# Kernel tuning notes

Hardware: AMD Instinct MI355X
Metric: run time of the kernel (lower is better)

## Reference

```python
import jax, jax.numpy as jnp
import numpy as np

N, C, E, H = 10000, 128, 640000, 8


def setup_inputs() -> dict:
    key = jax.random.key(0)
    k1, k2, k3, k4, k5 = jax.random.split(key, 5)
    x = jax.random.normal(k1, (N, C), dtype=jnp.float32)
    edge_index = jax.random.randint(k2, (2, E), 0, N, dtype=jnp.int64)
    edge_attr = jax.random.uniform(k3, (E,), dtype=jnp.float32)
    W = jax.random.normal(k4, (2 * C, H), dtype=jnp.float32) * (1.0 / np.sqrt(2 * C))
    b = jax.random.normal(k5, (H,), dtype=jnp.float32) * 0.01
    return {"x": x, "edge_index": edge_index, "edge_attr": edge_attr, "W": W, "b": b}


def reference(x, edge_index, edge_attr, W, b):
    row, col = edge_index[0], edge_index[1]
    # Split W so we never materialize the concatenated [E, 2C] tensor:
    # cat([x[row], x[col]]) @ W == x[row] @ W[:C] + x[col] @ W[C:]
    Wr, Wc = W[:x.shape[1]], W[x.shape[1]:]
    logits = x[row] @ Wr + x[col] @ Wc + b          # [E, H]
    alpha = jax.nn.sigmoid(logits) * edge_attr[:, None]
    self_loop = (row == col)[:, None]                # [E, 1] -> broadcast over heads
    alpha = jnp.where(self_loop, jnp.ones((), dtype=alpha.dtype), alpha)
    return (alpha, edge_index)
```

## Files before the change

kernel.cpp:

```cpp
#include <hip/hip_runtime.h>

#define N_NODES 10000
#define C_DIM   128
#define H_DIM   8

__global__ void precompute_yz(const float* __restrict__ x,
                              const float* __restrict__ W,
                              const float* __restrict__ b,
                              float* __restrict__ yz) {
    int idx = blockIdx.x * blockDim.x + threadIdx.x;
    const int total = N_NODES * H_DIM;
    if (idx >= total) return;
    int n = idx / H_DIM;
    int h = idx % H_DIM;
    const float* xr = x + n * C_DIM;
    float accr = 0.f, accc = 0.f;
#pragma unroll 8
    for (int k = 0; k < C_DIM; ++k) {
        float xv = xr[k];
        accr = fmaf(xv, W[k * H_DIM + h], accr);
        accc = fmaf(xv, W[(k + C_DIM) * H_DIM + h], accc);
    }
    yz[idx]         = accr + b[h];
    yz[total + idx] = accc;
}

__global__ void edge_alpha(const int* __restrict__ ei,
                           const float* __restrict__ ea,
                           const float* __restrict__ yz,
                           float* __restrict__ out, int E) {
    int e = blockIdx.x * blockDim.x + threadIdx.x;
    if (e >= E) return;
    int r = ei[e];
    int c = ei[E + e];
    float a = ea[e];

    const float4* yp = (const float4*)(yz + r * H_DIM);
    const float4* zp = (const float4*)(yz + N_NODES * H_DIM + c * H_DIM);
    float4 y0 = yp[0], y1 = yp[1];
    float4 z0 = zp[0], z1 = zp[1];

    float v[8] = { y0.x + z0.x, y0.y + z0.y, y0.z + z0.z, y0.w + z0.w,
                   y1.x + z1.x, y1.y + z1.y, y1.z + z1.z, y1.w + z1.w };
    bool self = (r == c);
    float res[8];
#pragma unroll
    for (int h = 0; h < 8; ++h) {
        float s = 1.f / (1.f + __expf(-v[h]));
        res[h] = self ? 1.f : s * a;
    }

    float4* op = (float4*)(out + (size_t)e * 8);
    op[0] = make_float4(res[0], res[1], res[2], res[3]);
    op[1] = make_float4(res[4], res[5], res[6], res[7]);

    out[(size_t)E * 8 + e]     = (float)r;
    out[(size_t)E * 8 + E + e] = (float)c;
}

extern "C" void kernel_launch(void* const* d_in, const int* in_sizes, int n_in,
                              void* d_out, int out_size, void* d_ws, size_t ws_size,
                              hipStream_t stream) {
    const float* x  = (const float*)d_in[0];
    const int*   ei = (const int*)d_in[1];
    const float* ea = (const float*)d_in[2];
    const float* W  = (const float*)d_in[3];
    const float* b  = (const float*)d_in[4];
    float* out = (float*)d_out;
    float* yz  = (float*)d_ws;

    const int E = in_sizes[2];

    {
        int total = N_NODES * H_DIM;
        int block = 256;
        int grid = (total + block - 1) / block;
        precompute_yz<<<grid, block, 0, stream>>>(x, W, b, yz);
    }
    {
        int block = 256;
        int grid = (E + block - 1) / block;
        edge_alpha<<<grid, block, 0, stream>>>(ei, ea, yz, out, E);
    }
}
```

Measured before the change: 26.96 us.

## Move edge-index conversion into precompute kernel and process two edges per thread

The int-to-float conversion of edge_index now runs as extra blocks of the first (precompute) kernel with int4/float4 vectorized accesses, so that write traffic overlaps with the node projection. The edge kernel then only writes alpha and handles two edges per thread to raise memory-level parallelism. The precompute loop also loads x as float4. The risk is that the pair-of-edges loads become less coalesced (stride 2 per thread) and the first kernel gets heavier.

```diff
diff --git a/kernel.cpp b/kernel.cpp
--- a/kernel.cpp
+++ b/kernel.cpp
@@ -1,61 +1,110 @@
 #include <hip/hip_runtime.h>
 
-#define N_NODES 10000
-#define C_DIM   128
-#define H_DIM   8
+#define N_NODES   10000
+#define C_DIM     128
+#define H_DIM     8
+#define BLOCK     256
+#define YZ_TOTAL  (N_NODES * H_DIM)
+#define YZ_BLOCKS ((YZ_TOTAL + BLOCK - 1) / BLOCK)
 
-__global__ void precompute_yz(const float* __restrict__ x,
-                              const float* __restrict__ W,
-                              const float* __restrict__ b,
-                              float* __restrict__ yz) {
-    int idx = blockIdx.x * blockDim.x + threadIdx.x;
-    const int total = N_NODES * H_DIM;
-    if (idx >= total) return;
-    int n = idx / H_DIM;
-    int h = idx % H_DIM;
-    const float* xr = x + n * C_DIM;
-    float accr = 0.f, accc = 0.f;
+__global__ void __launch_bounds__(BLOCK)
+k1_yz_and_index(const float* __restrict__ x,
+                const float* __restrict__ W,
+                const float* __restrict__ b,
+                const int*   __restrict__ ei,
+                float* __restrict__ out,
+                float* __restrict__ yz, int E) {
+    const int bid = blockIdx.x;
+
+    if (bid < YZ_BLOCKS) {
+        const int idx = bid * BLOCK + threadIdx.x;
+        if (idx < YZ_TOTAL) {
+            const int n = idx >> 3;
+            const int h = idx & 7;
+            const float4* xr4 = (const float4*)(x + (size_t)n * C_DIM);
+            const float* wr = W + h;
+            const float* wc = W + C_DIM * H_DIM + h;
+            float accr = 0.f, accc = 0.f;
 #pragma unroll 8
-    for (int k = 0; k < C_DIM; ++k) {
-        float xv = xr[k];
-        accr = fmaf(xv, W[k * H_DIM + h], accr);
-        accc = fmaf(xv, W[(k + C_DIM) * H_DIM + h], accc);
+            for (int kk = 0; kk < C_DIM / 4; ++kk) {
+                float4 xv = xr4[kk];
+                const int kb = kk * 4 * H_DIM;
+                accr = fmaf(xv.x, wr[kb],      accr);
+                accr = fmaf(xv.y, wr[kb + 8],  accr);
+                accr = fmaf(xv.z, wr[kb + 16], accr);
+                accr = fmaf(xv.w, wr[kb + 24], accr);
+                accc = fmaf(xv.x, wc[kb],      accc);
+                accc = fmaf(xv.y, wc[kb + 8],  accc);
+                accc = fmaf(xv.z, wc[kb + 16], accc);
+                accc = fmaf(xv.w, wc[kb + 24], accc);
+            }
+            yz[idx]            = accr + b[h];
+            yz[YZ_TOTAL + idx] = accc;
+        }
+    } else {
+        const size_t ib = (size_t)E * H_DIM;
+        const int t = (bid - YZ_BLOCKS) * BLOCK + threadIdx.x;
+        const int i = t * 4;
+        const int total = 2 * E;
+        if (i + 3 < total) {
+            int4 v = *(const int4*)(ei + i);
+            *(float4*)(out + ib + i) =
+                make_float4((float)v.x, (float)v.y, (float)v.z, (float)v.w);
+        } else {
+            for (int j = i; j < total; ++j) out[ib + j] = (float)ei[j];
+        }
     }
-    yz[idx]         = accr + b[h];
-    yz[total + idx] = accc;
 }
 
-__global__ void edge_alpha(const int* __restrict__ ei,
-                           const float* __restrict__ ea,
-                           const float* __restrict__ yz,
-                           float* __restrict__ out, int E) {
-    int e = blockIdx.x * blockDim.x + threadIdx.x;
+__global__ void __launch_bounds__(BLOCK)
+k2_edge_alpha(const int* __restrict__ ei,
+              const float* __restrict__ ea,
+              const float* __restrict__ yz,
+              float* __restrict__ out, int E) {
+    const int t = blockIdx.x * blockDim.x + threadIdx.x;
+    const int e = t * 2;
     if (e >= E) return;
-    int r = ei[e];
-    int c = ei[E + e];
-    float a = ea[e];
 
-    const float4* yp = (const float4*)(yz + r * H_DIM);
-    const float4* zp = (const float4*)(yz + N_NODES * H_DIM + c * H_DIM);
-    float4 y0 = yp[0], y1 = yp[1];
-    float4 z0 = zp[0], z1 = zp[1];
+    const bool two = (e + 1 < E);
+    int r0 = ei[e],     r1 = two ? ei[e + 1]     : 0;
+    int c0 = ei[E + e], c1 = two ? ei[E + e + 1] : 0;
+    float a0 = ea[e],   a1 = two ? ea[e + 1]     : 0.f;
 
-    float v[8] = { y0.x + z0.x, y0.y + z0.y, y0.z + z0.z, y0.w + z0.w,
-                   y1.x + z1.x, y1.y + z1.y, y1.z + z1.z, y1.w + z1.w };
-    bool self = (r == c);
-    float res[8];
+    const float* ybase = yz;
+    const float* zbase = yz + YZ_TOTAL;
+
+    const float4* yp0 = (const float4*)(ybase + (size_t)r0 * H_DIM);
+    const float4* zp0 = (const float4*)(zbase + (size_t)c0 * H_DIM);
+    const float4* yp1 = (const float4*)(ybase + (size_t)r1 * H_DIM);
+    const float4* zp1 = (const float4*)(zbase + (size_t)c1 * H_DIM);
+
+    float4 y00 = yp0[0], y01 = yp0[1], z00 = zp0[0], z01 = zp0[1];
+    float4 y10 = yp1[0], y11 = yp1[1], z10 = zp1[0], z11 = zp1[1];
+
+    float v0[8] = { y00.x + z00.x, y00.y + z00.y, y00.z + z00.z, y00.w + z00.w,
+                    y01.x + z01.x, y01.y + z01.y, y01.z + z01.z, y01.w + z01.w };
+    float v1[8] = { y10.x + z10.x, y10.y + z10.y, y10.z + z10.z, y10.w + z10.w,
+                    y11.x + z11.x, y11.y + z11.y, y11.z + z11.z, y11.w + z11.w };
+
+    const bool self0 = (r0 == c0);
+    const bool self1 = (r1 == c1);
+    float res0[8], res1[8];
 #pragma unroll
     for (int h = 0; h < 8; ++h) {
-        float s = 1.f / (1.f + __expf(-v[h]));
-        res[h] = self ? 1.f : s * a;
+        float s0 = 1.f / (1.f + __expf(-v0[h]));
+        float s1 = 1.f / (1.f + __expf(-v1[h]));
+        res0[h] = self0 ? 1.f : s0 * a0;
+        res1[h] = self1 ? 1.f : s1 * a1;
     }
 
-    float4* op = (float4*)(out + (size_t)e * 8);
-    op[0] = make_float4(res[0], res[1], res[2], res[3]);
-    op[1] = make_float4(res[4], res[5], res[6], res[7]);
-
-    out[(size_t)E * 8 + e]     = (float)r;
-    out[(size_t)E * 8 + E + e] = (float)c;
+    float4* op0 = (float4*)(out + (size_t)e * H_DIM);
+    op0[0] = make_float4(res0[0], res0[1], res0[2], res0[3]);
+    op0[1] = make_float4(res0[4], res0[5], res0[6], res0[7]);
+    if (two) {
+        float4* op1 = (float4*)(out + (size_t)(e + 1) * H_DIM);
+        op1[0] = make_float4(res1[0], res1[1], res1[2], res1[3]);
+        op1[1] = make_float4(res1[4], res1[5], res1[6], res1[7]);
+    }
 }
 
 extern "C" void kernel_launch(void* const* d_in, const int* in_sizes, int n_in,
@@ -68,18 +117,19 @@
     const float* b  = (const float*)d_in[4];
     float* out = (float*)d_out;
     float* yz  = (float*)d_ws;
-
     const int E = in_sizes[2];
 
     {
-        int total = N_NODES * H_DIM;
-        int block = 256;
-        int grid = (total + block - 1) / block;
-        precompute_yz<<<grid, block, 0, stream>>>(x, W, b, yz);
+        const int conv_threads = (2 * E + 3) / 4;
+        const int conv_blocks  = (conv_threads + BLOCK - 1) / BLOCK;
+        const int grid = YZ_BLOCKS + conv_blocks;
+        hipLaunchKernelGGL(k1_yz_and_index, dim3(grid), dim3(BLOCK), 0, stream,
+                           x, W, b, ei, out, yz, E);
     }
     {
-        int block = 256;
-        int grid = (E + block - 1) / block;
-        edge_alpha<<<grid, block, 0, stream>>>(ei, ea, yz, out, E);
+        const int threads = (E + 1) / 2;
+        const int grid = (threads + BLOCK - 1) / BLOCK;
+        hipLaunchKernelGGL(k2_edge_alpha, dim3(grid), dim3(BLOCK), 0, stream,
+                           ei, ea, yz, out, E);
     }
 }
```

New measurement: 27.88 us. +3.4%, slower.

## Split per-node projection across 32 lanes with vectorized loads and shuffle reduction

Applied to the files above, without the earlier changes.

The node projection kernel now assigns 32 threads per node: each lane handles a 16-element slice of the channel dimension for two heads, using float4 loads of x and float2 loads of W, then reduces partial sums with xor shuffles. This replaces the old one-thread-per-(node,head) serial 128-step loop, which made long dependent FMA chains and strided loads. The goal is more parallelism and shorter latency in the precompute stage, at the cost of shuffle work and more threads. The edge kernel changes only in index casts.

```diff
diff --git a/kernel.cpp b/kernel.cpp
--- a/kernel.cpp
+++ b/kernel.cpp
@@ -1,28 +1,56 @@
 #include <hip/hip_runtime.h>
 
-#define N_NODES 10000
-#define C_DIM   128
-#define H_DIM   8
+#define N_NODES  10000
+#define C_DIM    128
+#define H_DIM    8
+#define YZ_TOTAL (N_NODES * H_DIM)
 
-__global__ void precompute_yz(const float* __restrict__ x,
-                              const float* __restrict__ W,
-                              const float* __restrict__ b,
-                              float* __restrict__ yz) {
-    int idx = blockIdx.x * blockDim.x + threadIdx.x;
-    const int total = N_NODES * H_DIM;
-    if (idx >= total) return;
-    int n = idx / H_DIM;
-    int h = idx % H_DIM;
-    const float* xr = x + n * C_DIM;
-    float accr = 0.f, accc = 0.f;
-#pragma unroll 8
-    for (int k = 0; k < C_DIM; ++k) {
-        float xv = xr[k];
-        accr = fmaf(xv, W[k * H_DIM + h], accr);
-        accc = fmaf(xv, W[(k + C_DIM) * H_DIM + h], accc);
+__global__ void __launch_bounds__(256)
+precompute_yz(const float* __restrict__ x, const float* __restrict__ W,
+              const float* __restrict__ b, float* __restrict__ yz) {
+    const int t = blockIdx.x * blockDim.x + threadIdx.x;
+    const int n = t >> 5;
+    if (n >= N_NODES) return;
+    const int w  = t & 31;
+    const int s  = w >> 2;
+    const int hp = w & 3;
+    const int h0 = hp * 2;
+
+    const float4* xr4 = (const float4*)(x + (size_t)n * C_DIM) + s * 4;
+    float4 xv0 = xr4[0], xv1 = xr4[1], xv2 = xr4[2], xv3 = xr4[3];
+    const float xk[16] = { xv0.x,xv0.y,xv0.z,xv0.w, xv1.x,xv1.y,xv1.z,xv1.w,
+                           xv2.x,xv2.y,xv2.z,xv2.w, xv3.x,xv3.y,xv3.z,xv3.w };
+
+    const int k0 = s * 16;
+    const float* wr = W + (size_t)k0 * H_DIM + h0;
+    const float* wc = W + (size_t)(C_DIM + k0) * H_DIM + h0;
+
+    float ar0 = 0.f, ar1 = 0.f, ac0 = 0.f, ac1 = 0.f;
+#pragma unroll
+    for (int j = 0; j < 16; ++j) {
+        float2 wr2 = *(const float2*)(wr + j * H_DIM);
+        float2 wc2 = *(const float2*)(wc + j * H_DIM);
+        ar0 = fmaf(xk[j], wr2.x, ar0);
+        ar1 = fmaf(xk[j], wr2.y, ar1);
+        ac0 = fmaf(xk[j], wc2.x, ac0);
+        ac1 = fmaf(xk[j], wc2.y, ac1);
     }
-    yz[idx]         = accr + b[h];
-    yz[total + idx] = accc;
+
+#pragma unroll
+    for (int m = 4; m <= 16; m <<= 1) {
+        ar0 += __shfl_xor(ar0, m, 64);
+        ar1 += __shfl_xor(ar1, m, 64);
+        ac0 += __shfl_xor(ac0, m, 64);
+        ac1 += __shfl_xor(ac1, m, 64);
+    }
+
+    if (s == 0) {
+        float2 bb = *(const float2*)(b + h0);
+        *(float2*)(yz + (size_t)n * H_DIM + h0) =
+            make_float2(ar0 + bb.x, ar1 + bb.y);
+        *(float2*)(yz + YZ_TOTAL + (size_t)n * H_DIM + h0) =
+            make_float2(ac0, ac1);
+    }
 }
 
 __global__ void edge_alpha(const int* __restrict__ ei,
@@ -35,8 +63,8 @@
     int c = ei[E + e];
     float a = ea[e];
 
-    const float4* yp = (const float4*)(yz + r * H_DIM);
-    const float4* zp = (const float4*)(yz + N_NODES * H_DIM + c * H_DIM);
+    const float4* yp = (const float4*)(yz + (size_t)r * H_DIM);
+    const float4* zp = (const float4*)(yz + YZ_TOTAL + (size_t)c * H_DIM);
     float4 y0 = yp[0], y1 = yp[1];
     float4 z0 = zp[0], z1 = zp[1];
 
@@ -50,12 +78,12 @@
         res[h] = self ? 1.f : s * a;
     }
 
-    float4* op = (float4*)(out + (size_t)e * 8);
+    float4* op = (float4*)(out + (size_t)e * H_DIM);
     op[0] = make_float4(res[0], res[1], res[2], res[3]);
     op[1] = make_float4(res[4], res[5], res[6], res[7]);
 
-    out[(size_t)E * 8 + e]     = (float)r;
-    out[(size_t)E * 8 + E + e] = (float)c;
+    out[(size_t)E * H_DIM + e]     = (float)r;
+    out[(size_t)E * H_DIM + E + e] = (float)c;
 }
 
 extern "C" void kernel_launch(void* const* d_in, const int* in_sizes, int n_in,
@@ -68,18 +96,17 @@
     const float* b  = (const float*)d_in[4];
     float* out = (float*)d_out;
     float* yz  = (float*)d_ws;
-
     const int E = in_sizes[2];
 
     {
-        int total = N_NODES * H_DIM;
-        int block = 256;
-        int grid = (total + block - 1) / block;
-        precompute_yz<<<grid, block, 0, stream>>>(x, W, b, yz);
+        const int total_threads = N_NODES * 32;
+        const int grid = (total_threads + 255) / 256;
+        hipLaunchKernelGGL(precompute_yz, dim3(grid), dim3(256), 0, stream,
+                           x, W, b, yz);
     }
     {
-        int block = 256;
-        int grid = (E + block - 1) / block;
-        edge_alpha<<<grid, block, 0, stream>>>(ei, ea, yz, out, E);
+        const int grid = (E + 255) / 256;
+        hipLaunchKernelGGL(edge_alpha, dim3(grid), dim3(256), 0, stream,
+                           ei, ea, yz, out, E);
     }
 }
```

Measured after the change: 25.35 us. 6.0% less time.
